# Kernel tuning notes

Measured on AMD Instinct MI355X. Metric: run time of the kernel, lower is better.

## Reference

```python
import jax, jax.numpy as jnp
import numpy as np
import math

B, T, P, E, H = 4, 64, 256, 512, 8
D = E // H
LN_EPS = 1e-5


def setup_inputs() -> dict:
    key = jax.random.key(0)
    ks = jax.random.split(key, 6)
    s = 0.02  # weight init scale
    return {
        "x": jax.random.normal(ks[0], (B, T, P, E), jnp.float32),
        "Wq": jax.random.normal(ks[1], (E, E), jnp.float32) * s,
        "bq": jnp.zeros((E,), jnp.float32),
        "Wk": jax.random.normal(ks[2], (E, E), jnp.float32) * s,
        "bk": jnp.zeros((E,), jnp.float32),
        "Wv": jax.random.normal(ks[3], (E, E), jnp.float32) * s,
        "bv": jnp.zeros((E,), jnp.float32),
        "Wo": jax.random.normal(ks[4], (E, E), jnp.float32) * s,
        "bo": jnp.zeros((E,), jnp.float32),
        "ln_g": jnp.ones((E,), jnp.float32),
        "ln_b": jnp.zeros((E,), jnp.float32),
    }


def _proj(x, W, b):
    # torch nn.Linear: y = x @ W.T + b
    return jnp.einsum('btpe,fe->btpf', x, W) + b


def _heads(y):
    # b t p (h d) -> b p h t d
    b, t, p, e = y.shape
    return y.reshape(b, t, p, H, D).transpose(0, 2, 3, 1, 4)


def reference(x, Wq, bq, Wk, bk, Wv, bv, Wo, bo, ln_g, ln_b):
    b, t, p, e = x.shape
    q = _heads(_proj(x, Wq, bq))  # [B,P,H,T,D]
    k = _heads(_proj(x, Wk, bk))
    v = _heads(_proj(x, Wv, bv))

    scores = jnp.einsum('bphtd,bphsd->bphts', q, k) / math.sqrt(D)
    causal_mask = jnp.triu(jnp.ones((t, t), dtype=bool), k=1)  # True above diag
    scores = jnp.where(causal_mask, -jnp.inf, scores)
    attn = jax.nn.softmax(scores, axis=-1)
    o = jnp.einsum('bphts,bphsd->bphtd', attn, v)

    # b p h t d -> b t p (h d)
    o = o.transpose(0, 3, 1, 2, 4).reshape(b, t, p, e)
    attn_out = jnp.einsum('btpe,fe->btpf', o, Wo) + bo

    y = x + attn_out
    # AdaptiveNormalizer with conditioning=None -> plain LayerNorm over E
    mu = jnp.mean(y, axis=-1, keepdims=True)
    var = jnp.var(y, axis=-1, keepdims=True)
    return (y - mu) * jax.lax.rsqrt(var + LN_EPS) * ln_g + ln_b
```

## Files before the change

kernel.cpp:

```cpp
#include <hip/hip_runtime.h>
#include <stdint.h>

#define B_ 4
#define T_ 64
#define P_ 256
#define E_ 512
#define H_ 8
#define D_ 64
#define NF 1536
#define MCH 16384

typedef unsigned short u16;
typedef __attribute__((ext_vector_type(8))) __bf16 bf16x8;
typedef __attribute__((ext_vector_type(4))) float f32x4;

__device__ __forceinline__ u16 f2bf(float x) {
  union { float f; uint32_t u; } a; a.f = x;
  uint32_t u = a.u;
  uint32_t r = (u + 0x7FFFu + ((u >> 16) & 1u)) >> 16;
  return (u16)r;
}

__device__ __forceinline__ bf16x8 ld8(const u16* p) {
  union { uint4 u; bf16x8 b; } t;
  t.u = *reinterpret_cast<const uint4*>(p);
  return t.b;
}

typedef __attribute__((address_space(3))) void lds_void;
typedef __attribute__((address_space(1))) void g_void;
__device__ __forceinline__ void gl_lds16(const void* g, void* l) {
  __builtin_amdgcn_global_load_lds((g_void*)g, (lds_void*)l, 16, 0, 0);
}

__device__ __forceinline__ f32x4 mfma16(bf16x8 a, bf16x8 b, f32x4 c) {
  return __builtin_amdgcn_mfma_f32_16x16x32_bf16(a, b, c, 0, 0, 0);
}

#define SBAR() __builtin_amdgcn_s_barrier()

__global__ void cvt_bf16(const float* __restrict__ src, u16* __restrict__ dst, int n8) {
  int i = blockIdx.x * blockDim.x + threadIdx.x;
  if (i >= n8) return;
  const float4* s = reinterpret_cast<const float4*>(src) + (size_t)i * 2;
  float4 a = s[0], b = s[1];
  union { u16 u[8]; uint4 v; } t;
  t.u[0] = f2bf(a.x); t.u[1] = f2bf(a.y); t.u[2] = f2bf(a.z); t.u[3] = f2bf(a.w);
  t.u[4] = f2bf(b.x); t.u[5] = f2bf(b.y); t.u[6] = f2bf(b.z); t.u[7] = f2bf(b.w);
  reinterpret_cast<uint4*>(dst)[i] = t.v;
}

__global__ void cvt_w(const float* __restrict__ Wq, const float* __restrict__ Wk,
                      const float* __restrict__ Wv, const float* __restrict__ Wo,
                      u16* __restrict__ wqkv, u16* __restrict__ wobf) {
  int idx = blockIdx.x * blockDim.x + threadIdx.x;
  int w = idx >> 15;
  int off = idx & 32767;
  const float* s = (w == 0) ? Wq : (w == 1) ? Wk : (w == 2) ? Wv : Wo;
  const float4* sp = reinterpret_cast<const float4*>(s) + (size_t)off * 2;
  float4 a = sp[0], b = sp[1];
  union { u16 u[8]; uint4 v; } t;
  t.u[0] = f2bf(a.x); t.u[1] = f2bf(a.y); t.u[2] = f2bf(a.z); t.u[3] = f2bf(a.w);
  t.u[4] = f2bf(b.x); t.u[5] = f2bf(b.y); t.u[6] = f2bf(b.z); t.u[7] = f2bf(b.w);
  if (w < 3) reinterpret_cast<uint4*>(wqkv)[w * 32768 + off] = t.v;
  else       reinterpret_cast<uint4*>(wobf)[off] = t.v;
}

#define K1_MFMA(MB)                                                         \
  __builtin_amdgcn_s_setprio(1);                                            \
  _Pragma("unroll") for (int i = 0; i < 4; i++)                             \
  _Pragma("unroll") for (int j = 0; j < 4; j++)                             \
    acc[(MB) + i][j] = mfma16(af[i], bfv[j], acc[(MB) + i][j]);             \
  __builtin_amdgcn_s_setprio(0);

#define K1_READA(E, HH, MB)                                                 \
  _Pragma("unroll") for (int i = 0; i < 4; i++)                             \
    af[i] = ld8(ldsA + ((E) * 2 + (HH)) * 8192 +                            \
                (wr * 128 + ((MB) + i) * 16 + l15) * 32 + xr8);

#define K1_READB(E, HH)                                                     \
  _Pragma("unroll") for (int j = 0; j < 4; j++)                             \
    bfv[j] = ld8(ldsB + ((E) * 2 + (HH)) * 8192 +                           \
                 (wc * 64 + j * 16 + l15) * 32 + xr8);

__global__ __launch_bounds__(512, 2) void k1_qkv(
    const u16* __restrict__ xbf,
    const u16* __restrict__ wqkv,
    const float* __restrict__ bq, const float* __restrict__ bk, const float* __restrict__ bv,
    u16* __restrict__ qkv)
{
  __shared__ u16 lds[65536];
  u16* ldsA = lds;
  u16* ldsB = lds + 32768;

  const int tid = threadIdx.x;
  const int lane = tid & 63, wid = tid >> 6;
  const int wr = wid >> 2, wc = wid & 3;
  const int g4 = lane >> 4, l15 = lane & 15;
  const int xr8 = (g4 ^ ((l15 >> 1) & 3)) * 8;

  const int cpx = gridDim.x >> 3;
  const int logical = (blockIdx.x & 7) * cpx + (blockIdx.x >> 3);
  const int m0 = (logical / 6) * 256;
  const int n0 = (logical % 6) * 256;

  const u16* ga = xbf + (size_t)m0 * E_;
  const u16* gb = wqkv + (size_t)n0 * E_;

  const int r0 = tid >> 2;
  const int c0 = ((tid & 3) ^ ((tid >> 3) & 3)) * 8;

  auto stageA = [&](int e, int h, int kt) {
    const int kc = kt * 64 + h * 32;
    u16* base = ldsA + (e * 2 + h) * 8192;
    gl_lds16(ga + (size_t)r0 * E_ + kc + c0, base + wid * 512);
    gl_lds16(ga + (size_t)(r0 + 128) * E_ + kc + c0, base + 4096 + wid * 512);
  };
  auto stageB = [&](int e, int h, int kt) {
    const int kc = kt * 64 + h * 32;
    u16* base = ldsB + (e * 2 + h) * 8192;
    gl_lds16(gb + (size_t)r0 * E_ + kc + c0, base + wid * 512);
    gl_lds16(gb + (size_t)(r0 + 128) * E_ + kc + c0, base + 4096 + wid * 512);
  };

  f32x4 acc[8][4];
#pragma unroll
  for (int i = 0; i < 8; i++)
#pragma unroll
    for (int j = 0; j < 4; j++) { f32x4 z = {0.f, 0.f, 0.f, 0.f}; acc[i][j] = z; }

  stageA(0, 0, 0); stageB(0, 0, 0);
  stageA(0, 1, 0); stageB(0, 1, 0);
  stageA(1, 0, 1); stageB(1, 0, 1);
  asm volatile("s_waitcnt vmcnt(8)" ::: "memory");
  SBAR();

#pragma unroll 2
  for (int s = 0; s < 8; ++s) {
    const int e = s & 1;
    bf16x8 af[4], bfv[4];
    K1_READA(e, 0, 0)
    K1_READB(e, 0)
    if (s < 7) stageA(e ^ 1, 1, s + 1);
    SBAR();
    K1_MFMA(0)
    SBAR();
    K1_READA(e, 0, 4)
    if (s < 7) stageB(e ^ 1, 1, s + 1);
    if (s < 7) { asm volatile("s_waitcnt vmcnt(8)" ::: "memory"); }
    else       { asm volatile("s_waitcnt vmcnt(0)" ::: "memory"); }
    SBAR();
    K1_MFMA(4)
    SBAR();
    K1_READA(e, 1, 0)
    K1_READB(e, 1)
    if (s < 6) stageA(e, 0, s + 2);
    SBAR();
    K1_MFMA(0)
    SBAR();
    K1_READA(e, 1, 4)
    if (s < 6) stageB(e, 0, s + 2);
    if (s < 6)      { asm volatile("s_waitcnt vmcnt(8)" ::: "memory"); }
    else if (s == 6){ asm volatile("s_waitcnt vmcnt(4)" ::: "memory"); }
    SBAR();
    K1_MFMA(4)
    SBAR();
  }

  float bias4[4];
#pragma unroll
  for (int ni = 0; ni < 4; ni++) {
    const int fcol = n0 + wc * 64 + ni * 16 + l15;
    bias4[ni] = fcol < 512 ? bq[fcol] : (fcol < 1024 ? bk[fcol - 512] : bv[fcol - 1024]);
  }
  const int fbase = n0 + wc * 64 + l15;
#pragma unroll
  for (int mi = 0; mi < 8; mi++)
#pragma unroll
    for (int r = 0; r < 4; r++) {
      const size_t row = m0 + wr * 128 + mi * 16 + g4 * 4 + r;
      u16* dst = qkv + row * NF + fbase;
#pragma unroll
      for (int ni = 0; ni < 4; ni++)
        dst[ni * 16] = f2bf(acc[mi][ni][r] + bias4[ni]);
    }
}

__global__ __launch_bounds__(256) void k2_attn(
    const u16* __restrict__ qkv,
    u16* __restrict__ o)
{
  __shared__ u16 Pl[4][64 * 72];
  const int tid = threadIdx.x, lane = tid & 63, wid = tid >> 6;
  const int gw = blockIdx.x * 4 + wid;
  const int b = gw >> 11;
  const int g = gw & 2047;
  const int h = g & 7, p = g >> 3;
  const int g4 = lane >> 4;
  const size_t ts = (size_t)P_ * NF;
  const u16* qb = qkv + (size_t)b * MCH * NF + (size_t)p * NF + h * D_;
  const u16* kb = qb + 512;
  const u16* vb = qb + 1024;
  u16* ob = o + (size_t)b * MCH * E_;

  bf16x8 qf[4][2], kf[4][2];
#pragma unroll
  for (int i = 0; i < 4; i++)
#pragma unroll
    for (int ks = 0; ks < 2; ks++) {
      const int rr = i * 16 + (lane & 15);
      const int dc = ks * 32 + g4 * 8;
      qf[i][ks] = ld8(qb + (size_t)rr * ts + dc);
      kf[i][ks] = ld8(kb + (size_t)rr * ts + dc);
    }
  f32x4 S[4][4];
#pragma unroll
  for (int i = 0; i < 4; i++)
#pragma unroll
    for (int j = 0; j < 4; j++) { f32x4 z = {0.f, 0.f, 0.f, 0.f}; S[i][j] = z; }
#pragma unroll
  for (int ks = 0; ks < 2; ks++)
#pragma unroll
    for (int mi = 0; mi < 4; mi++)
#pragma unroll
      for (int ni = 0; ni < 4; ni++)
        S[mi][ni] = mfma16(qf[mi][ks], kf[ni][ks], S[mi][ni]);

  u16* pw = &Pl[wid][0];
#pragma unroll
  for (int mi = 0; mi < 4; mi++)
#pragma unroll
    for (int r = 0; r < 4; r++) {
      const int t = mi * 16 + g4 * 4 + r;
      float v[4]; float mx = -1e30f;
#pragma unroll
      for (int ni = 0; ni < 4; ni++) {
        const int s = ni * 16 + (lane & 15);
        v[ni] = (s <= t) ? S[mi][ni][r] * 0.125f : -1e30f;
        mx = fmaxf(mx, v[ni]);
      }
      mx = fmaxf(mx, __shfl_xor(mx, 1));
      mx = fmaxf(mx, __shfl_xor(mx, 2));
      mx = fmaxf(mx, __shfl_xor(mx, 4));
      mx = fmaxf(mx, __shfl_xor(mx, 8));
      float sum = 0.f; float pv[4];
#pragma unroll
      for (int ni = 0; ni < 4; ni++) {
        const int s = ni * 16 + (lane & 15);
        pv[ni] = (s <= t) ? __expf(v[ni] - mx) : 0.f;
        sum += pv[ni];
      }
      sum += __shfl_xor(sum, 1);
      sum += __shfl_xor(sum, 2);
      sum += __shfl_xor(sum, 4);
      sum += __shfl_xor(sum, 8);
      const float inv = 1.0f / sum;
#pragma unroll
      for (int ni = 0; ni < 4; ni++) {
        const int s = ni * 16 + (lane & 15);
        pw[t * 72 + s] = f2bf(pv[ni] * inv);
      }
    }
  __syncthreads();

  f32x4 O[4][4];
#pragma unroll
  for (int i = 0; i < 4; i++)
#pragma unroll
    for (int j = 0; j < 4; j++) { f32x4 z = {0.f, 0.f, 0.f, 0.f}; O[i][j] = z; }
#pragma unroll
  for (int ks = 0; ks < 2; ks++) {
    bf16x8 pa[4], vf[4];
#pragma unroll
    for (int mi = 0; mi < 4; mi++)
      pa[mi] = ld8(pw + (mi * 16 + (lane & 15)) * 72 + ks * 32 + g4 * 8);
#pragma unroll
    for (int ni = 0; ni < 4; ni++) {
      union { u16 u[8]; bf16x8 b; } tv;
#pragma unroll
      for (int j = 0; j < 8; j++) {
        const int s = ks * 32 + g4 * 8 + j;
        tv.u[j] = vb[(size_t)s * ts + ni * 16 + (lane & 15)];
      }
      vf[ni] = tv.b;
    }
#pragma unroll
    for (int mi = 0; mi < 4; mi++)
#pragma unroll
      for (int ni = 0; ni < 4; ni++)
        O[mi][ni] = mfma16(pa[mi], vf[ni], O[mi][ni]);
  }
#pragma unroll
  for (int mi = 0; mi < 4; mi++)
#pragma unroll
    for (int ni = 0; ni < 4; ni++)
#pragma unroll
      for (int r = 0; r < 4; r++) {
        const int t = mi * 16 + g4 * 4 + r;
        const int d = ni * 16 + (lane & 15);
        ob[((size_t)t * P_ + p) * E_ + h * D_ + d] = f2bf(O[mi][ni][r]);
      }
}

__global__ __launch_bounds__(512, 2) void k3_out(
    const u16* __restrict__ obf,
    const u16* __restrict__ wo,
    const float* __restrict__ bo,
    const float* __restrict__ x,
    const float* __restrict__ lng, const float* __restrict__ lnb,
    float* __restrict__ out)
{
  __shared__ float redS[64][8];
  __shared__ float redQ[64][8];
  const int tid = threadIdx.x, lane = tid & 63, wid = tid >> 6;
  const int g4 = lane >> 4, l15 = lane & 15;
  const int m0 = blockIdx.x * 64;

  const u16* ga = obf + (size_t)m0 * E_;
  const u16* gb = wo + (size_t)(wid * 64) * E_;

  f32x4 acc[4][4];
#pragma unroll
  for (int i = 0; i < 4; i++)
#pragma unroll
    for (int j = 0; j < 4; j++) { f32x4 z = {0.f, 0.f, 0.f, 0.f}; acc[i][j] = z; }

  bf16x8 afA[4][2], afB[4][2], bfA[4][2], bfB[4][2];

#define K3_LOADA(AF, T)                                                     \
  _Pragma("unroll") for (int mi = 0; mi < 4; mi++)                          \
  _Pragma("unroll") for (int ks = 0; ks < 2; ks++)                          \
    AF[mi][ks] = ld8(ga + (size_t)(mi * 16 + l15) * E_ + (T) * 64 + ks * 32 + g4 * 8);
#define K3_LOADB(BF, T)                                                     \
  _Pragma("unroll") for (int ni = 0; ni < 4; ni++)                          \
  _Pragma("unroll") for (int ks = 0; ks < 2; ks++)                          \
    BF[ni][ks] = ld8(gb + (size_t)(ni * 16 + l15) * E_ + (T) * 64 + ks * 32 + g4 * 8);
#define K3_COMP(AF, BF)                                                     \
  _Pragma("unroll") for (int ks = 0; ks < 2; ks++)                          \
  _Pragma("unroll") for (int mi = 0; mi < 4; mi++)                          \
  _Pragma("unroll") for (int ni = 0; ni < 4; ni++)                          \
    acc[mi][ni] = mfma16(AF[mi][ks], BF[ni][ks], acc[mi][ni]);

  K3_LOADA(afA, 0)
  K3_LOADB(bfA, 0)
#pragma unroll
  for (int t = 0; t < 8; t += 2) {
    if (t + 1 < 8) { K3_LOADA(afB, t + 1) K3_LOADB(bfB, t + 1) }
    K3_COMP(afA, bfA)
    if (t + 2 < 8) { K3_LOADA(afA, t + 2) K3_LOADB(bfA, t + 2) }
    if (t + 1 < 8) { K3_COMP(afB, bfB) }
  }

  const int fb = wid * 64 + l15;
  float gg[4], bb[4], bof[4];
#pragma unroll
  for (int ni = 0; ni < 4; ni++) {
    const int f = fb + ni * 16;
    gg[ni] = lng[f]; bb[ni] = lnb[f]; bof[ni] = bo[f];
  }
#pragma unroll
  for (int mi = 0; mi < 4; mi++)
#pragma unroll
    for (int r = 0; r < 4; r++) {
      const int n = m0 + mi * 16 + g4 * 4 + r;
#pragma unroll
      for (int ni = 0; ni < 4; ni++)
        acc[mi][ni][r] += bof[ni] + x[(size_t)n * E_ + fb + ni * 16];
    }
#pragma unroll
  for (int mi = 0; mi < 4; mi++)
#pragma unroll
    for (int r = 0; r < 4; r++) {
      float s = 0.f, q = 0.f;
#pragma unroll
      for (int ni = 0; ni < 4; ni++) { const float y = acc[mi][ni][r]; s += y; q += y * y; }
      s += __shfl_xor(s, 1); q += __shfl_xor(q, 1);
      s += __shfl_xor(s, 2); q += __shfl_xor(q, 2);
      s += __shfl_xor(s, 4); q += __shfl_xor(q, 4);
      s += __shfl_xor(s, 8); q += __shfl_xor(q, 8);
      if (l15 == 0) {
        const int rl = mi * 16 + g4 * 4 + r;
        redS[rl][wid] = s; redQ[rl][wid] = q;
      }
    }
  __syncthreads();
#pragma unroll
  for (int mi = 0; mi < 4; mi++)
#pragma unroll
    for (int r = 0; r < 4; r++) {
      const int rl = mi * 16 + g4 * 4 + r;
      float Sx = 0.f, Qx = 0.f;
#pragma unroll
      for (int w = 0; w < 8; w++) { Sx += redS[rl][w]; Qx += redQ[rl][w]; }
      const float mean = Sx * (1.0f / 512.0f);
      const float var = Qx * (1.0f / 512.0f) - mean * mean;
      const float rs = rsqrtf(var + 1e-5f);
      const int n = m0 + rl;
#pragma unroll
      for (int ni = 0; ni < 4; ni++)
        out[(size_t)n * E_ + fb + ni * 16] = (acc[mi][ni][r] - mean) * rs * gg[ni] + bb[ni];
    }
}

extern "C" void kernel_launch(void* const* d_in, const int* in_sizes, int n_in,
                              void* d_out, int out_size, void* d_ws, size_t ws_size,
                              hipStream_t stream) {
  const float* x   = (const float*)d_in[0];
  const float* Wq  = (const float*)d_in[1];
  const float* bq  = (const float*)d_in[2];
  const float* Wk  = (const float*)d_in[3];
  const float* bk  = (const float*)d_in[4];
  const float* Wv  = (const float*)d_in[5];
  const float* bv  = (const float*)d_in[6];
  const float* Wo  = (const float*)d_in[7];
  const float* bo  = (const float*)d_in[8];
  const float* lng = (const float*)d_in[9];
  const float* lnb = (const float*)d_in[10];
  float* out = (float*)d_out;
  uint8_t* ws = (uint8_t*)d_ws;

  const size_t NEED_BIG = 270532608ULL;
  if (ws_size >= NEED_BIG) {
    u16* wqkv = (u16*)(ws);
    u16* wobf = (u16*)(ws + 1572864);
    u16* xbf  = (u16*)(ws + 2097152);
    u16* qkvc = (u16*)(ws + 69206016);
    u16* obf  = xbf;

    cvt_w<<<512, 256, 0, stream>>>(Wq, Wk, Wv, Wo, wqkv, wobf);
    cvt_bf16<<<16384, 256, 0, stream>>>(x, xbf, B_ * MCH * E_ / 8);
    k1_qkv<<<1536, 512, 0, stream>>>(xbf, wqkv, bq, bk, bv, qkvc);
    k2_attn<<<2048, 256, 0, stream>>>(qkvc, obf);
    k3_out<<<1024, 512, 0, stream>>>(obf, wobf, bo, x, lng, lnb, out);
  } else {
    u16* xbf  = (u16*)(ws);
    u16* qkvc = (u16*)(ws + 16777216);
    u16* obf  = (u16*)(ws + 67108864);
    u16* wqkv = (u16*)(ws + 83886080);
    u16* wobf = (u16*)(ws + 85458944);

    cvt_w<<<512, 256, 0, stream>>>(Wq, Wk, Wv, Wo, wqkv, wobf);
    for (int b = 0; b < B_; ++b) {
      const float* xb = x + (size_t)b * MCH * E_;
      cvt_bf16<<<4096, 256, 0, stream>>>(xb, xbf, MCH * E_ / 8);
      k1_qkv<<<384, 512, 0, stream>>>(xbf, wqkv, bq, bk, bv, qkvc);
      k2_attn<<<512, 256, 0, stream>>>(qkvc, obf);
      k3_out<<<256, 512, 0, stream>>>(obf, wobf, bo, xb, lng, lnb, out + (size_t)b * MCH * E_);
    }
  }
}
```

Before: 398.3 us.

## Split output projection into LDS-pipelined GEMM plus separate LayerNorm kernel

Replaces the direct-from-global output projection (64-row tiles, fused LayerNorm) with the k1-style LDS double-buffered 256x256 GEMM that writes a bf16 residual sum, followed by a standalone row-wise LayerNorm kernel. The aim is better operand reuse and MFMA efficiency in the Wo GEMM. The cost is an extra bf16 round-trip of the full activation tensor and one more launch. Storing y in bf16 before normalization also adds rounding error.

```diff
diff --git a/kernel.cpp b/kernel.cpp
--- a/kernel.cpp
+++ b/kernel.cpp
@@ -66,22 +66,59 @@
   else       reinterpret_cast<uint4*>(wobf)[off] = t.v;
 }
 
-#define K1_MFMA(MB)                                                         \
+#define GP_MFMA(MB)                                                         \
   __builtin_amdgcn_s_setprio(1);                                            \
   _Pragma("unroll") for (int i = 0; i < 4; i++)                             \
   _Pragma("unroll") for (int j = 0; j < 4; j++)                             \
     acc[(MB) + i][j] = mfma16(af[i], bfv[j], acc[(MB) + i][j]);             \
   __builtin_amdgcn_s_setprio(0);
 
-#define K1_READA(E, HH, MB)                                                 \
+#define GP_READA(E, HH, MB)                                                 \
   _Pragma("unroll") for (int i = 0; i < 4; i++)                             \
     af[i] = ld8(ldsA + ((E) * 2 + (HH)) * 8192 +                            \
                 (wr * 128 + ((MB) + i) * 16 + l15) * 32 + xr8);
 
-#define K1_READB(E, HH)                                                     \
+#define GP_READB(E, HH)                                                     \
   _Pragma("unroll") for (int j = 0; j < 4; j++)                             \
     bfv[j] = ld8(ldsB + ((E) * 2 + (HH)) * 8192 +                           \
                  (wc * 64 + j * 16 + l15) * 32 + xr8);
+
+#define GP_KLOOP()                                                          \
+  stageA(0, 0, 0); stageB(0, 0, 0);                                         \
+  stageA(0, 1, 0); stageB(0, 1, 0);                                         \
+  stageA(1, 0, 1); stageB(1, 0, 1);                                         \
+  asm volatile("s_waitcnt vmcnt(8)" ::: "memory");                          \
+  SBAR();                                                                   \
+  _Pragma("unroll 2") for (int s = 0; s < 8; ++s) {                         \
+    const int e = s & 1;                                                    \
+    bf16x8 af[4], bfv[4];                                                   \
+    GP_READA(e, 0, 0)                                                       \
+    GP_READB(e, 0)                                                          \
+    if (s < 7) stageA(e ^ 1, 1, s + 1);                                     \
+    SBAR();                                                                 \
+    GP_MFMA(0)                                                              \
+    SBAR();                                                                 \
+    GP_READA(e, 0, 4)                                                       \
+    if (s < 7) stageB(e ^ 1, 1, s + 1);                                     \
+    if (s < 7) { asm volatile("s_waitcnt vmcnt(8)" ::: "memory"); }         \
+    else       { asm volatile("s_waitcnt vmcnt(0)" ::: "memory"); }         \
+    SBAR();                                                                 \
+    GP_MFMA(4)                                                              \
+    SBAR();                                                                 \
+    GP_READA(e, 1, 0)                                                       \
+    GP_READB(e, 1)                                                          \
+    if (s < 6) stageA(e, 0, s + 2);                                         \
+    SBAR();                                                                 \
+    GP_MFMA(0)                                                              \
+    SBAR();                                                                 \
+    GP_READA(e, 1, 4)                                                       \
+    if (s < 6) stageB(e, 0, s + 2);                                         \
+    if (s < 6)      { asm volatile("s_waitcnt vmcnt(8)" ::: "memory"); }    \
+    else if (s == 6){ asm volatile("s_waitcnt vmcnt(4)" ::: "memory"); }    \
+    SBAR();                                                                 \
+    GP_MFMA(4)                                                              \
+    SBAR();                                                                 \
+  }
 
 __global__ __launch_bounds__(512, 2) void k1_qkv(
     const u16* __restrict__ xbf,
@@ -129,43 +166,7 @@
 #pragma unroll
     for (int j = 0; j < 4; j++) { f32x4 z = {0.f, 0.f, 0.f, 0.f}; acc[i][j] = z; }
 
-  stageA(0, 0, 0); stageB(0, 0, 0);
-  stageA(0, 1, 0); stageB(0, 1, 0);
-  stageA(1, 0, 1); stageB(1, 0, 1);
-  asm volatile("s_waitcnt vmcnt(8)" ::: "memory");
-  SBAR();
-
-#pragma unroll 2
-  for (int s = 0; s < 8; ++s) {
-    const int e = s & 1;
-    bf16x8 af[4], bfv[4];
-    K1_READA(e, 0, 0)
-    K1_READB(e, 0)
-    if (s < 7) stageA(e ^ 1, 1, s + 1);
-    SBAR();
-    K1_MFMA(0)
-    SBAR();
-    K1_READA(e, 0, 4)
-    if (s < 7) stageB(e ^ 1, 1, s + 1);
-    if (s < 7) { asm volatile("s_waitcnt vmcnt(8)" ::: "memory"); }
-    else       { asm volatile("s_waitcnt vmcnt(0)" ::: "memory"); }
-    SBAR();
-    K1_MFMA(4)
-    SBAR();
-    K1_READA(e, 1, 0)
-    K1_READB(e, 1)
-    if (s < 6) stageA(e, 0, s + 2);
-    SBAR();
-    K1_MFMA(0)
-    SBAR();
-    K1_READA(e, 1, 4)
-    if (s < 6) stageB(e, 0, s + 2);
-    if (s < 6)      { asm volatile("s_waitcnt vmcnt(8)" ::: "memory"); }
-    else if (s == 6){ asm volatile("s_waitcnt vmcnt(4)" ::: "memory"); }
-    SBAR();
-    K1_MFMA(4)
-    SBAR();
-  }
+  GP_KLOOP()
 
   float bias4[4];
 #pragma unroll
@@ -302,104 +303,104 @@
       }
 }
 
-__global__ __launch_bounds__(512, 2) void k3_out(
+__global__ __launch_bounds__(512, 2) void k3_gemm(
     const u16* __restrict__ obf,
     const u16* __restrict__ wo,
     const float* __restrict__ bo,
     const float* __restrict__ x,
-    const float* __restrict__ lng, const float* __restrict__ lnb,
-    float* __restrict__ out)
+    u16* __restrict__ yb)
 {
-  __shared__ float redS[64][8];
-  __shared__ float redQ[64][8];
-  const int tid = threadIdx.x, lane = tid & 63, wid = tid >> 6;
+  __shared__ u16 lds[65536];
+  u16* ldsA = lds;
+  u16* ldsB = lds + 32768;
+
+  const int tid = threadIdx.x;
+  const int lane = tid & 63, wid = tid >> 6;
+  const int wr = wid >> 2, wc = wid & 3;
   const int g4 = lane >> 4, l15 = lane & 15;
-  const int m0 = blockIdx.x * 64;
+  const int xr8 = (g4 ^ ((l15 >> 1) & 3)) * 8;
+
+  const int cpx = gridDim.x >> 3;
+  const int logical = (blockIdx.x & 7) * cpx + (blockIdx.x >> 3);
+  const int m0 = (logical >> 1) * 256;
+  const int n0 = (logical & 1) * 256;
 
   const u16* ga = obf + (size_t)m0 * E_;
-  const u16* gb = wo + (size_t)(wid * 64) * E_;
-
-  f32x4 acc[4][4];
-#pragma unroll
-  for (int i = 0; i < 4; i++)
+  const u16* gb = wo + (size_t)n0 * E_;
+
+  const int r0 = tid >> 2;
+  const int c0 = ((tid & 3) ^ ((tid >> 3) & 3)) * 8;
+
+  auto stageA = [&](int e, int h, int kt) {
+    const int kc = kt * 64 + h * 32;
+    u16* base = ldsA + (e * 2 + h) * 8192;
+    gl_lds16(ga + (size_t)r0 * E_ + kc + c0, base + wid * 512);
+    gl_lds16(ga + (size_t)(r0 + 128) * E_ + kc + c0, base + 4096 + wid * 512);
+  };
+  auto stageB = [&](int e, int h, int kt) {
+    const int kc = kt * 64 + h * 32;
+    u16* base = ldsB + (e * 2 + h) * 8192;
+    gl_lds16(gb + (size_t)r0 * E_ + kc + c0, base + wid * 512);
+    gl_lds16(gb + (size_t)(r0 + 128) * E_ + kc + c0, base + 4096 + wid * 512);
+  };
+
+  f32x4 acc[8][4];
+#pragma unroll
+  for (int i = 0; i < 8; i++)
 #pragma unroll
     for (int j = 0; j < 4; j++) { f32x4 z = {0.f, 0.f, 0.f, 0.f}; acc[i][j] = z; }
 
-  bf16x8 afA[4][2], afB[4][2], bfA[4][2], bfB[4][2];
-
-#define K3_LOADA(AF, T)                                                     \
-  _Pragma("unroll") for (int mi = 0; mi < 4; mi++)                          \
-  _Pragma("unroll") for (int ks = 0; ks < 2; ks++)                          \
-    AF[mi][ks] = ld8(ga + (size_t)(mi * 16 + l15) * E_ + (T) * 64 + ks * 32 + g4 * 8);
-#define K3_LOADB(BF, T)                                                     \
-  _Pragma("unroll") for (int ni = 0; ni < 4; ni++)                          \
-  _Pragma("unroll") for (int ks = 0; ks < 2; ks++)                          \
-    BF[ni][ks] = ld8(gb + (size_t)(ni * 16 + l15) * E_ + (T) * 64 + ks * 32 + g4 * 8);
-#define K3_COMP(AF, BF)                                                     \
-  _Pragma("unroll") for (int ks = 0; ks < 2; ks++)                          \
-  _Pragma("unroll") for (int mi = 0; mi < 4; mi++)                          \
-  _Pragma("unroll") for (int ni = 0; ni < 4; ni++)                          \
-    acc[mi][ni] = mfma16(AF[mi][ks], BF[ni][ks], acc[mi][ni]);
-
-  K3_LOADA(afA, 0)
-  K3_LOADB(bfA, 0)
-#pragma unroll
-  for (int t = 0; t < 8; t += 2) {
-    if (t + 1 < 8) { K3_LOADA(afB, t + 1) K3_LOADB(bfB, t + 1) }
-    K3_COMP(afA, bfA)
-    if (t + 2 < 8) { K3_LOADA(afA, t + 2) K3_LOADB(bfA, t + 2) }
-    if (t + 1 < 8) { K3_COMP(afB, bfB) }
+  GP_KLOOP()
+
+  float bias4[4];
+#pragma unroll
+  for (int ni = 0; ni < 4; ni++)
+    bias4[ni] = bo[n0 + wc * 64 + ni * 16 + l15];
+  const int fbase = n0 + wc * 64 + l15;
+#pragma unroll
+  for (int mi = 0; mi < 8; mi++)
+#pragma unroll
+    for (int r = 0; r < 4; r++) {
+      const size_t row = m0 + wr * 128 + mi * 16 + g4 * 4 + r;
+      u16* dst = yb + row * E_ + fbase;
+      const float* xr = x + row * E_ + fbase;
+#pragma unroll
+      for (int ni = 0; ni < 4; ni++)
+        dst[ni * 16] = f2bf(acc[mi][ni][r] + bias4[ni] + xr[ni * 16]);
+    }
+}
+
+__global__ __launch_bounds__(256) void k3_ln(
+    const u16* __restrict__ yb, const float* __restrict__ lng,
+    const float* __restrict__ lnb, float* __restrict__ out)
+{
+  const int lane = threadIdx.x & 63;
+  const size_t row = (size_t)blockIdx.x * 4 + (threadIdx.x >> 6);
+  const int c = lane * 8;
+  const uint4 d = *reinterpret_cast<const uint4*>(yb + row * E_ + c);
+  const uint32_t* dw = reinterpret_cast<const uint32_t*>(&d);
+  float f[8];
+#pragma unroll
+  for (int j = 0; j < 4; j++) {
+    union { uint32_t u; float v; } lo, hi;
+    lo.u = dw[j] << 16; hi.u = dw[j] & 0xffff0000u;
+    f[2 * j] = lo.v; f[2 * j + 1] = hi.v;
   }
-
-  const int fb = wid * 64 + l15;
-  float gg[4], bb[4], bof[4];
-#pragma unroll
-  for (int ni = 0; ni < 4; ni++) {
-    const int f = fb + ni * 16;
-    gg[ni] = lng[f]; bb[ni] = lnb[f]; bof[ni] = bo[f];
-  }
-#pragma unroll
-  for (int mi = 0; mi < 4; mi++)
-#pragma unroll
-    for (int r = 0; r < 4; r++) {
-      const int n = m0 + mi * 16 + g4 * 4 + r;
-#pragma unroll
-      for (int ni = 0; ni < 4; ni++)
-        acc[mi][ni][r] += bof[ni] + x[(size_t)n * E_ + fb + ni * 16];
-    }
-#pragma unroll
-  for (int mi = 0; mi < 4; mi++)
-#pragma unroll
-    for (int r = 0; r < 4; r++) {
-      float s = 0.f, q = 0.f;
-#pragma unroll
-      for (int ni = 0; ni < 4; ni++) { const float y = acc[mi][ni][r]; s += y; q += y * y; }
-      s += __shfl_xor(s, 1); q += __shfl_xor(q, 1);
-      s += __shfl_xor(s, 2); q += __shfl_xor(q, 2);
-      s += __shfl_xor(s, 4); q += __shfl_xor(q, 4);
-      s += __shfl_xor(s, 8); q += __shfl_xor(q, 8);
-      if (l15 == 0) {
-        const int rl = mi * 16 + g4 * 4 + r;
-        redS[rl][wid] = s; redQ[rl][wid] = q;
-      }
-    }
-  __syncthreads();
-#pragma unroll
-  for (int mi = 0; mi < 4; mi++)
-#pragma unroll
-    for (int r = 0; r < 4; r++) {
-      const int rl = mi * 16 + g4 * 4 + r;
-      float Sx = 0.f, Qx = 0.f;
-#pragma unroll
-      for (int w = 0; w < 8; w++) { Sx += redS[rl][w]; Qx += redQ[rl][w]; }
-      const float mean = Sx * (1.0f / 512.0f);
-      const float var = Qx * (1.0f / 512.0f) - mean * mean;
-      const float rs = rsqrtf(var + 1e-5f);
-      const int n = m0 + rl;
-#pragma unroll
-      for (int ni = 0; ni < 4; ni++)
-        out[(size_t)n * E_ + fb + ni * 16] = (acc[mi][ni][r] - mean) * rs * gg[ni] + bb[ni];
-    }
+  float s = 0.f, q = 0.f;
+#pragma unroll
+  for (int j = 0; j < 8; j++) { s += f[j]; q += f[j] * f[j]; }
+#pragma unroll
+  for (int d2 = 1; d2 < 64; d2 <<= 1) { s += __shfl_xor(s, d2); q += __shfl_xor(q, d2); }
+  const float mean = s * (1.0f / 512.0f);
+  const float var = q * (1.0f / 512.0f) - mean * mean;
+  const float rs = rsqrtf(var + 1e-5f);
+  float o8[8];
+#pragma unroll
+  for (int j = 0; j < 8; j++)
+    o8[j] = (f[j] - mean) * rs * lng[c + j] + lnb[c + j];
+  float4* op = reinterpret_cast<float4*>(out + row * E_ + c);
+  op[0] = make_float4(o8[0], o8[1], o8[2], o8[3]);
+  op[1] = make_float4(o8[4], o8[5], o8[6], o8[7]);
 }
 
 extern "C" void kernel_launch(void* const* d_in, const int* in_sizes, int n_in,
@@ -426,18 +427,21 @@
     u16* xbf  = (u16*)(ws + 2097152);
     u16* qkvc = (u16*)(ws + 69206016);
     u16* obf  = xbf;
+    u16* yb   = qkvc;
 
     cvt_w<<<512, 256, 0, stream>>>(Wq, Wk, Wv, Wo, wqkv, wobf);
     cvt_bf16<<<16384, 256, 0, stream>>>(x, xbf, B_ * MCH * E_ / 8);
     k1_qkv<<<1536, 512, 0, stream>>>(xbf, wqkv, bq, bk, bv, qkvc);
     k2_attn<<<2048, 256, 0, stream>>>(qkvc, obf);
-    k3_out<<<1024, 512, 0, stream>>>(obf, wobf, bo, x, lng, lnb, out);
+    k3_gemm<<<512, 512, 0, stream>>>(obf, wobf, bo, x, yb);
+    k3_ln<<<16384, 256, 0, stream>>>(yb, lng, lnb, out);
   } else {
     u16* xbf  = (u16*)(ws);
     u16* qkvc = (u16*)(ws + 16777216);
     u16* obf  = (u16*)(ws + 67108864);
     u16* wqkv = (u16*)(ws + 83886080);
     u16* wobf = (u16*)(ws + 85458944);
+    u16* yb   = qkvc;
 
     cvt_w<<<512, 256, 0, stream>>>(Wq, Wk, Wv, Wo, wqkv, wobf);
     for (int b = 0; b < B_; ++b) {
@@ -445,7 +449,8 @@
       cvt_bf16<<<4096, 256, 0, stream>>>(xb, xbf, MCH * E_ / 8);
       k1_qkv<<<384, 512, 0, stream>>>(xbf, wqkv, bq, bk, bv, qkvc);
       k2_attn<<<512, 256, 0, stream>>>(qkvc, obf);
-      k3_out<<<256, 512, 0, stream>>>(obf, wobf, bo, xb, lng, lnb, out + (size_t)b * MCH * E_);
+      k3_gemm<<<128, 512, 0, stream>>>(obf, wobf, bo, xb, yb);
+      k3_ln<<<4096, 256, 0, stream>>>(yb, lng, lnb, out + (size_t)b * MCH * E_);
     }
   }
 }
```

Result: faster. 361.1 us (-9.3%).
